# Optimization experiments

Measured on AMD Instinct MI355X. Metric: run time of the kernel, lower is better.

Reference implementation:

```python
import jax, jax.numpy as jnp
import numpy as np

N_NODES = 10000
N_EDGES = 80000
D = 512
L = 5
ALPHA = 0.1  # LeakyReLU slope inside GraphAttention
ACT_ALPHA = 0.1  # outer activation slope
EPS = 1e-5
W_SCALE = 0.05  # ~ xavier_normal gain 1.414 for fan_in+fan_out=1536


def leaky(x, a):
    return jnp.where(x >= 0, x, a * x)


def setup_inputs() -> dict:
    key = jax.random.key(0)
    ks = jax.random.split(key, 9)
    return {
        "node_feats": jax.random.normal(ks[0], (N_NODES, D), jnp.float32),
        "edge_feats": jax.random.normal(ks[1], (N_EDGES, D), jnp.float32),
        "src": jax.random.randint(ks[2], (N_EDGES,), 0, N_NODES, jnp.int32),
        "dst": jax.random.randint(ks[3], (N_EDGES,), 0, N_NODES, jnp.int32),
        "Wa": jax.random.normal(ks[4], (L, 2 * D, D), jnp.float32) * W_SCALE,
        "Wn": jax.random.normal(ks[5], (L, 2 * D, D), jnp.float32) * W_SCALE,
        "We": jax.random.normal(ks[6], (L, 2 * D, D), jnp.float32) * W_SCALE,
        "Wnc": jax.random.normal(ks[7], (D, 55), jnp.float32) * W_SCALE,
        "Wec": jax.random.normal(ks[8], (D, 2), jnp.float32) * W_SCALE,
    }


def reference(node_feats, edge_feats, src, dst, Wa, Wn, We, Wnc, Wec):
    n = node_feats.shape[0]
    nx, ex = node_feats, edge_feats
    for l in range(L):
        nx_src = nx[src]  # [E, D]
        nx_dst = nx[dst]  # [E, D]
        # a_p = exp(fa([e_x, dst_x]) - columnwise max over edges)
        ap = jnp.concatenate((ex, nx_dst), axis=1) @ Wa[l]
        ap = jnp.exp(ap - jnp.max(ap, axis=0, keepdims=True))
        # a_r = exp(fa([e_x, src_x]) - columnwise max over edges)
        ar = jnp.concatenate((ex, nx_src), axis=1) @ Wa[l]
        ar = jnp.exp(ar - jnp.max(ar, axis=0, keepdims=True))
        # softmax-like normalization per destination node
        z = jax.ops.segment_sum(ap, dst, num_segments=n)  # [N, D]
        a = ap / (z[dst] + EPS)
        # aggregate a * edge_x to destination nodes
        z2 = jax.ops.segment_sum(a * ex, dst, num_segments=n)  # [N, D]
        ft = jnp.concatenate((z2, nx), axis=1) @ Wn[l]
        # edge update: blend src/dst node feats by a_r/a_p shares
        a_sum = ap + ar
        blend = (ar / a_sum) * nx_src + (ap / a_sum) * nx_dst
        ex_new = jnp.concatenate((blend, ex), axis=1) @ We[l]
        # inner leaky_relu then outer activation (both LeakyReLU)
        nx = leaky(leaky(ft, ALPHA), ACT_ALPHA)
        ex = leaky(leaky(ex_new, ALPHA), ACT_ALPHA)
    node_conf = nx @ Wnc
    edge_conf = ex @ Wec
    return (nx, node_conf, ex, edge_conf)
```

## Files before the change

kernel.cpp:

```cpp
#include <hip/hip_runtime.h>
#include <hip/hip_fp16.h>
#include <math.h>

#define D 512
#define NNODES 10000
#define NEDGES 80000
#define LAYERS 5
#define EPS 1e-5f

typedef _Float16 f16x8 __attribute__((ext_vector_type(8)));
typedef float f32x4 __attribute__((ext_vector_type(4)));

__device__ inline unsigned short f2h(float x) { return __half_as_ushort(__float2half(x)); }
__device__ inline float h2f(unsigned short u) { return __half2float(__ushort_as_half(u)); }
__device__ inline uint4 pack8(const unsigned short* v) {
  uint4 r;
  r.x = (unsigned)v[0] | ((unsigned)v[1] << 16);
  r.y = (unsigned)v[2] | ((unsigned)v[3] << 16);
  r.z = (unsigned)v[4] | ((unsigned)v[5] << 16);
  r.w = (unsigned)v[6] | ((unsigned)v[7] << 16);
  return r;
}
__device__ inline void unpack8(uint4 v, unsigned short* o) {
  o[0] = v.x & 0xffff; o[1] = v.x >> 16;
  o[2] = v.y & 0xffff; o[3] = v.y >> 16;
  o[4] = v.z & 0xffff; o[5] = v.z >> 16;
  o[6] = v.w & 0xffff; o[7] = v.w >> 16;
}

__device__ inline void gload16(const void* g, void* l) {
  __builtin_amdgcn_global_load_lds((const __attribute__((address_space(1))) void*)g,
                                   (__attribute__((address_space(3))) void*)l, 16, 0, 0);
}

__device__ inline int octA(int r, int o) {
  return ((o >> 2) << 6) + ((((o & 3) ^ ((r >> 1) & 3))) << 4);
}

__global__ __launch_bounds__(256) void toF16_k(const float* __restrict__ src,
                                               char* __restrict__ dst, int nOct) {
  for (long long i = (long long)blockIdx.x * 256 + threadIdx.x; i < nOct;
       i += (long long)gridDim.x * 256) {
    int row = (int)(i >> 6), oct = (int)(i & 63);
    const float* s = src + (size_t)row * 512 + oct * 8;
    float4 x0 = *(const float4*)s, x1 = *(const float4*)(s + 4);
    float xs[8] = {x0.x, x0.y, x0.z, x0.w, x1.x, x1.y, x1.z, x1.w};
    unsigned short h[8];
#pragma unroll
    for (int j = 0; j < 8; j++) h[j] = f2h(xs[j]);
    *(uint4*)(dst + (size_t)row * 1024 + octA(row, oct)) = pack8(h);
  }
}

__global__ __launch_bounds__(256) void wprep_k(const float* __restrict__ Wa,
                                               const float* __restrict__ Wn,
                                               const float* __restrict__ We,
                                               char* __restrict__ WT) {
  __shared__ float tile[64][65];
  int mat = blockIdx.z;
  const float* W = (mat < 5) ? Wa + (size_t)mat * 1024 * 512
                 : (mat < 10) ? Wn + (size_t)(mat - 5) * 1024 * 512
                              : We + (size_t)(mat - 10) * 1024 * 512;
  char* out = WT + (size_t)mat * 512 * 2048;
  int n0 = blockIdx.x * 64, k0 = blockIdx.y * 64;
  int t = threadIdx.x;
  int ty = t >> 2, tx = t & 3;
  const float* wr = W + (size_t)(k0 + ty) * 512 + n0 + tx * 16;
  float4 v0 = *(const float4*)(wr + 0), v1 = *(const float4*)(wr + 4);
  float4 v2 = *(const float4*)(wr + 8), v3 = *(const float4*)(wr + 12);
  float vv[16] = {v0.x, v0.y, v0.z, v0.w, v1.x, v1.y, v1.z, v1.w,
                  v2.x, v2.y, v2.z, v2.w, v3.x, v3.y, v3.z, v3.w};
#pragma unroll
  for (int j = 0; j < 16; j++) tile[ty][tx * 16 + j] = vv[j];
  __syncthreads();
#pragma unroll
  for (int p = 0; p < 2; p++) {
    int chunk = t + p * 256;
    int n = chunk >> 3, cc = chunk & 7;
    float xs[8];
#pragma unroll
    for (int j = 0; j < 8; j++) xs[j] = tile[cc * 8 + j][n];
    unsigned short h[8];
#pragma unroll
    for (int j = 0; j < 8; j++) h[j] = f2h(xs[j]);
    int ng = n0 + n;
    int kc = (k0 >> 3) + cc;
    *(uint4*)(out + (size_t)ng * 2048 + octA(ng, kc)) = pack8(h);
  }
}

__global__ __launch_bounds__(256) void hist_k(const int* __restrict__ dst, int* __restrict__ cnt) {
  int e = blockIdx.x * 256 + threadIdx.x;
  if (e < NEDGES) atomicAdd(&cnt[dst[e]], 1);
}

__global__ __launch_bounds__(256) void scan_k(const int* __restrict__ cnt,
                                              int* __restrict__ off, int* __restrict__ cur) {
  __shared__ int part[256];
  const int CH = (NNODES + 255) / 256;
  int t = threadIdx.x;
  int s = 0;
  int l0 = t * CH;
  for (int i = 0; i < CH; i++) {
    int idx = l0 + i;
    if (idx < NNODES) s += cnt[idx];
  }
  part[t] = s;
  __syncthreads();
  if (t == 0) {
    int acc = 0;
    for (int i = 0; i < 256; i++) { int v = part[i]; part[i] = acc; acc += v; }
  }
  __syncthreads();
  int acc = part[t];
  for (int i = 0; i < CH; i++) {
    int idx = l0 + i;
    if (idx < NNODES) { off[idx] = acc; cur[idx] = acc; acc += cnt[idx]; }
  }
  if (t == 255) off[NNODES] = acc;
}

__global__ __launch_bounds__(256) void scatter_k(const int* __restrict__ dst,
                                                 int* __restrict__ cur, int* __restrict__ eid) {
  int e = blockIdx.x * 256 + threadIdx.x;
  if (e < NEDGES) {
    int p = atomicAdd(&cur[dst[e]], 1);
    eid[p] = e;
  }
}

template<int KT, bool ACT, bool OUT_I, bool CMAX>
__global__ __launch_bounds__(256) void gemmI(const char* __restrict__ X1,
                                             const char* __restrict__ X2,
                                             const char* __restrict__ BW, int cb0,
                                             void* __restrict__ Yout, int R,
                                             const int* __restrict__ srcI,
                                             const int* __restrict__ dstI,
                                             const float* __restrict__ Na,
                                             float* __restrict__ part_p,
                                             float* __restrict__ part_r) {
  __shared__ char smem[49152];
  const int tid = threadIdx.x;
  const int lane = tid & 63, wv = tid >> 6;
  const int NT = KT / 32;
  int flat = blockIdx.y * 4 + blockIdx.x;
  int total = gridDim.y * 4;
  int xcd = flat & 7, idx = flat >> 3;
  int q = total >> 3, rem = total & 7;
  int base = xcd * q + (xcd < rem ? xcd : rem);
  int f2 = base + idx;
  const int bn0 = (f2 & 3) * 128, bm0 = (f2 >> 2) * 128;
  const int r16 = lane & 15, g = lane >> 4;
  const int mo = (wv >> 1) * 64, no = (wv & 1) * 64;
  const int lr16 = lane >> 2, ls16 = (lane & 3) * 16;
  f32x4 acc[4][4];
#pragma unroll
  for (int i = 0; i < 4; i++)
#pragma unroll
    for (int j = 0; j < 4; j++) acc[i][j] = (f32x4){0.f, 0.f, 0.f, 0.f};

  int offA[4], offB[4];
#pragma unroll
  for (int mi = 0; mi < 4; mi++) {
    int row = mo + mi * 16 + r16;
    offA[mi] = row * 64 + ((g ^ ((row >> 1) & 3)) << 4);
  }
#pragma unroll
  for (int ni = 0; ni < 4; ni++) {
    int row = no + ni * 16 + r16;
    offB[ni] = row * 64 + ((g ^ ((row >> 1) & 3)) << 4);
  }

  const char* pA0;
  const char* pA1;
  const char* pB0;
  const char* pB1;
  {
    int g0 = bm0 + wv * 16 + lr16; if (g0 > R - 1) g0 = R - 1;
    int g1 = bm0 + (4 + wv) * 16 + lr16; if (g1 > R - 1) g1 = R - 1;
    pA0 = X1 + (size_t)g0 * 1024 + ls16;
    pA1 = X1 + (size_t)g1 * 1024 + ls16;
    int n0r = bn0 + wv * 16 + lr16;
    int n1r = bn0 + (4 + wv) * 16 + lr16;
    pB0 = BW + (size_t)n0r * 2048 + cb0 * 16 + ls16;
    pB1 = BW + (size_t)n1r * 2048 + cb0 * 16 + ls16;
  }

  int us = 0;
#define STAGE()                                                 \
  {                                                             \
    char* sb = smem + (us % 3) * 16384;                         \
    gload16(pA0, sb + wv * 1024);                               \
    gload16(pA1, sb + (4 + wv) * 1024);                         \
    gload16(pB0, sb + 8192 + wv * 1024);                        \
    gload16(pB1, sb + 8192 + (4 + wv) * 1024);                  \
    pA0 += 64; pA1 += 64; pB0 += 64; pB1 += 64;                 \
    us++;                                                       \
  }

  STAGE();
  STAGE();
  for (int t = 0; t < NT; ++t) {
    if (t + 1 < NT) {
      asm volatile("s_waitcnt vmcnt(4)" ::: "memory");
    } else {
      asm volatile("s_waitcnt vmcnt(0)" ::: "memory");
    }
    __builtin_amdgcn_s_barrier();
    if (us < NT) {
      if (KT == 1024 && us == 16) {
        int g0 = bm0 + wv * 16 + lr16; if (g0 > R - 1) g0 = R - 1;
        int g1 = bm0 + (4 + wv) * 16 + lr16; if (g1 > R - 1) g1 = R - 1;
        pA0 = X2 + (size_t)g0 * 1024 + ls16;
        pA1 = X2 + (size_t)g1 * 1024 + ls16;
      }
      STAGE();
    }
    const char* As = smem + (t % 3) * 16384;
    const char* Bs = As + 8192;
    f16x8 a[4], b[4];
#pragma unroll
    for (int mi = 0; mi < 4; mi++) a[mi] = *(const f16x8*)(As + offA[mi]);
#pragma unroll
    for (int ni = 0; ni < 4; ni++) b[ni] = *(const f16x8*)(Bs + offB[ni]);
    __builtin_amdgcn_s_setprio(1);
#pragma unroll
    for (int mi = 0; mi < 4; mi++)
#pragma unroll
      for (int ni = 0; ni < 4; ni++)
        acc[mi][ni] = __builtin_amdgcn_mfma_f32_16x16x32_f16(a[mi], b[ni], acc[mi][ni], 0, 0, 0);
    __builtin_amdgcn_s_setprio(0);
  }
#undef STAGE

  if (!OUT_I) {
    float* Y = (float*)Yout;
#pragma unroll
    for (int mi = 0; mi < 4; mi++)
#pragma unroll
      for (int j = 0; j < 4; j++) {
        int row = bm0 + mo + mi * 16 + g * 4 + j;
        if (row < R) {
#pragma unroll
          for (int ni = 0; ni < 4; ni++) {
            float v = acc[mi][ni][j];
            if (ACT) v = (v >= 0.f) ? v : 0.01f * v;
            Y[(size_t)row * 512 + bn0 + no + ni * 16 + r16] = v;
          }
        }
      }
  } else {
    float* stg = (float*)smem;
    const int rg = tid >> 5, cq = (tid & 31) * 4;
    float4 mp4 = make_float4(-1e30f, -1e30f, -1e30f, -1e30f);
    float4 mr4 = mp4;
#pragma unroll
    for (int h = 0; h < 2; h++) {
      __syncthreads();
      if ((wv >> 1) == h) {
#pragma unroll
        for (int mi = 0; mi < 4; mi++)
#pragma unroll
          for (int j = 0; j < 4; j++) {
            int rl = mi * 16 + g * 4 + j;
#pragma unroll
            for (int ni = 0; ni < 4; ni++) {
              float v = acc[mi][ni][j];
              if (ACT) v = (v >= 0.f) ? v : 0.01f * v;
              stg[rl * 128 + no + ni * 16 + r16] = v;
            }
          }
      }
      __syncthreads();
#pragma unroll
      for (int qq = 0; qq < 4; qq++) {
        int idx2 = tid + qq * 256;
        int rl = idx2 >> 4, oc = idx2 & 15;
        int grow = bm0 + h * 64 + rl;
        if (grow < R) {
          unsigned short hh[8];
#pragma unroll
          for (int j = 0; j < 8; j++) hh[j] = f2h(stg[rl * 128 + oc * 8 + j]);
          int oct = (bn0 >> 3) + oc;
          *(uint4*)((char*)Yout + (size_t)grow * 1024 + octA(grow, oct)) = pack8(hh);
        }
      }
      if (CMAX) {
#pragma unroll 2
        for (int r = rg * 8; r < rg * 8 + 8; r++) {
          int grow = bm0 + h * 64 + r;
          int d = dstI[grow], s = srcI[grow];
          float4 v = *(const float4*)&stg[r * 128 + cq];
          v.x = h2f(f2h(v.x)); v.y = h2f(f2h(v.y));
          v.z = h2f(f2h(v.z)); v.w = h2f(f2h(v.w));
          float4 nd = *(const float4*)&Na[(size_t)d * 512 + bn0 + cq];
          float4 ns = *(const float4*)&Na[(size_t)s * 512 + bn0 + cq];
          mp4.x = fmaxf(mp4.x, v.x + nd.x); mp4.y = fmaxf(mp4.y, v.y + nd.y);
          mp4.z = fmaxf(mp4.z, v.z + nd.z); mp4.w = fmaxf(mp4.w, v.w + nd.w);
          mr4.x = fmaxf(mr4.x, v.x + ns.x); mr4.y = fmaxf(mr4.y, v.y + ns.y);
          mr4.z = fmaxf(mr4.z, v.z + ns.z); mr4.w = fmaxf(mr4.w, v.w + ns.w);
        }
      }
    }
    if (CMAX) {
      __syncthreads();
      float* red = (float*)smem;
      *(float4*)&red[rg * 128 + cq] = mp4;
      *(float4*)&red[1024 + rg * 128 + cq] = mr4;
      __syncthreads();
      if (tid < 128) {
        float vp = -1e30f, vr = -1e30f;
#pragma unroll
        for (int gi = 0; gi < 8; gi++) {
          vp = fmaxf(vp, red[gi * 128 + tid]);
          vr = fmaxf(vr, red[1024 + gi * 128 + tid]);
        }
        int panel = f2 >> 2;
        part_p[(size_t)panel * 512 + bn0 + tid] = vp;
        part_r[(size_t)panel * 512 + bn0 + tid] = vr;
      }
    }
  }
}

__global__ __launch_bounds__(256) void colmax_red_k(const float* __restrict__ part,
                                                    float* __restrict__ m) {
  int idx = blockIdx.x * 256 + threadIdx.x;
  int c = idx & 511;
  const float* P = part + (size_t)(idx >> 9) * (625 * 512) + c;
  float v = -1e30f;
#pragma unroll 1
  for (int b = 0; b < 625; b += 5) {
    float v0 = P[(size_t)(b + 0) * 512], v1 = P[(size_t)(b + 1) * 512];
    float v2 = P[(size_t)(b + 2) * 512], v3 = P[(size_t)(b + 3) * 512];
    float v4 = P[(size_t)(b + 4) * 512];
    v = fmaxf(v, fmaxf(fmaxf(v0, v1), fmaxf(fmaxf(v2, v3), v4)));
  }
  m[idx] = v;
}

__global__ __launch_bounds__(256) void aggblend_k(const char* __restrict__ EaH,
                                                  const float* __restrict__ Na,
                                                  const char* __restrict__ exI,
                                                  const char* __restrict__ nxI,
                                                  const int* __restrict__ src,
                                                  const int* __restrict__ off,
                                                  const int* __restrict__ eid,
                                                  const float* __restrict__ mp,
                                                  const float* __restrict__ mr,
                                                  char* __restrict__ blendH,
                                                  char* __restrict__ z2I) {
  const int w = threadIdx.x >> 6, o = threadIdx.x & 63;
  int n = blockIdx.x * 4 + w;
  if (n >= NNODES) return;
  float m_p[8], m_r[8], nd[8], xd[8], z[8], z2[8];
#pragma unroll
  for (int j = 0; j < 8; j++) {
    m_p[j] = mp[o * 8 + j];
    m_r[j] = mr[o * 8 + j];
    z[j] = 0.f; z2[j] = 0.f;
  }
  {
    const float* np = Na + (size_t)n * 512 + o * 8;
    float4 d0 = *(const float4*)np, d1 = *(const float4*)(np + 4);
    nd[0] = d0.x; nd[1] = d0.y; nd[2] = d0.z; nd[3] = d0.w;
    nd[4] = d1.x; nd[5] = d1.y; nd[6] = d1.z; nd[7] = d1.w;
    unsigned short hh[8];
    unpack8(*(const uint4*)(nxI + (size_t)n * 1024 + octA(n, o)), hh);
#pragma unroll
    for (int j = 0; j < 8; j++) xd[j] = h2f(hh[j]);
  }
  const int i0 = off[n], i1 = off[n + 1];
  if (i0 < i1) {
    int e = eid[i0];
    int s = src[e];
    uint4 cea = *(const uint4*)(EaH + (size_t)e * 1024 + octA(e, o));
    const float* ns = Na + (size_t)s * 512 + o * 8;
    float4 cs0 = *(const float4*)ns, cs1 = *(const float4*)(ns + 4);
    uint4 cx = *(const uint4*)(exI + (size_t)e * 1024 + octA(e, o));
    uint4 cn = *(const uint4*)(nxI + (size_t)s * 1024 + octA(s, o));
    for (int i = i0; i < i1; i++) {
      int en = 0, sn = 0;
      float4 ps0, ps1;
      uint4 pea, px, pn;
      const bool more = (i + 1 < i1);
      if (more) {
        en = eid[i + 1];
        sn = src[en];
        pea = *(const uint4*)(EaH + (size_t)en * 1024 + octA(en, o));
        const float* ns2 = Na + (size_t)sn * 512 + o * 8;
        ps0 = *(const float4*)ns2; ps1 = *(const float4*)(ns2 + 4);
        px = *(const uint4*)(exI + (size_t)en * 1024 + octA(en, o));
        pn = *(const uint4*)(nxI + (size_t)sn * 1024 + octA(sn, o));
      }
      unsigned short eh[8], xh[8], sh[8];
      unpack8(cea, eh);
      unpack8(cx, xh);
      unpack8(cn, sh);
      float sv[8] = {cs0.x, cs0.y, cs0.z, cs0.w, cs1.x, cs1.y, cs1.z, cs1.w};
      unsigned short bh[8];
#pragma unroll
      for (int j = 0; j < 8; j++) {
        float ev = h2f(eh[j]);
        float sp = ev + nd[j] - m_p[j];
        float sr = ev + sv[j] - m_r[j];
        float ap = __expf(sp);
        float xe = h2f(xh[j]);
        z[j] += ap;
        z2[j] += ap * xe;
        float u = sr - sp;
        float evx = __expf(-fabsf(u));
        float wpos = 1.f / (1.f + evx);
        float wr = (u >= 0.f) ? wpos : 1.f - wpos;
        float xs_ = h2f(sh[j]);
        bh[j] = f2h(wr * xs_ + (1.f - wr) * xd[j]);
      }
      *(uint4*)(blendH + (size_t)e * 1024 + octA(e, o)) = pack8(bh);
      if (more) {
        e = en; s = sn;
        cea = pea; cs0 = ps0; cs1 = ps1;
        cx = px; cn = pn;
      }
    }
  }
  unsigned short zh[8];
#pragma unroll
  for (int j = 0; j < 8; j++) zh[j] = f2h(z2[j] / (z[j] + EPS));
  *(uint4*)(z2I + (size_t)n * 1024 + octA(n, o)) = pack8(zh);
}

__global__ __launch_bounds__(256) void nodeconf_k(const float* __restrict__ nx,
                                                  const float* __restrict__ Wnc,
                                                  float* __restrict__ out) {
  int w = threadIdx.x >> 6, lane = threadIdx.x & 63;
  int n = blockIdx.x * 4 + w;
  const float* r = nx + (size_t)n * D;
  if (lane < 55) {
    float acc = 0.f;
    for (int k = 0; k < D; k++) acc = fmaf(r[k], Wnc[k * 55 + lane], acc);
    out[(size_t)n * 55 + lane] = acc;
  }
}

__global__ __launch_bounds__(256) void edgeconf_k(const float* __restrict__ ex,
                                                  const float* __restrict__ Wec,
                                                  float* __restrict__ out) {
  int w = threadIdx.x >> 6, lane = threadIdx.x & 63;
  int e = blockIdx.x * 4 + w;
  const float* r = ex + (size_t)e * D;
  float a0 = 0.f, a1 = 0.f;
#pragma unroll
  for (int j = 0; j < 8; j++) {
    int c = lane + j * 64;
    float x = r[c];
    a0 = fmaf(x, Wec[c * 2 + 0], a0);
    a1 = fmaf(x, Wec[c * 2 + 1], a1);
  }
#pragma unroll
  for (int off = 32; off; off >>= 1) {
    a0 += __shfl_down(a0, off);
    a1 += __shfl_down(a1, off);
  }
  if (lane == 0) { out[(size_t)e * 2 + 0] = a0; out[(size_t)e * 2 + 1] = a1; }
}

extern "C" void kernel_launch(void* const* d_in, const int* in_sizes, int n_in,
                              void* d_out, int out_size, void* d_ws, size_t ws_size,
                              hipStream_t stream) {
  const float* in_nx = (const float*)d_in[0];
  const float* in_ex = (const float*)d_in[1];
  const int* src = (const int*)d_in[2];
  const int* dst = (const int*)d_in[3];
  const float* Wa = (const float*)d_in[4];
  const float* Wn = (const float*)d_in[5];
  const float* We = (const float*)d_in[6];
  const float* Wnc = (const float*)d_in[7];
  const float* Wec = (const float*)d_in[8];

  float* out = (float*)d_out;
  float* o_nx = out;
  float* o_nc = o_nx + (size_t)NNODES * D;
  float* o_ex = o_nc + (size_t)NNODES * 55;
  float* o_ec = o_ex + (size_t)NEDGES * D;

  const size_t SZ_EH = (size_t)NEDGES * 1024;
  const size_t SZ_NH = (size_t)NNODES * 1024;
  const size_t SZ_NF = (size_t)NNODES * 2048;
  const size_t MATSZ = (size_t)512 * 2048;
  char* w = (char*)d_ws;
  char* EaH = w;
  char* blendH = w + SZ_EH;
  char* exA = w + 2 * SZ_EH;
  char* nxA = w + 3 * SZ_EH;
  float* Na = (float*)(w + 3 * SZ_EH + SZ_NH);
  char* z2I = w + 3 * SZ_EH + SZ_NH + SZ_NF;
  float* mpf = (float*)(w + 3 * SZ_EH + 2 * SZ_NH + SZ_NF);
  char* WT = w + 3 * SZ_EH + 2 * SZ_NH + SZ_NF + 8192;
  char* csr = WT + 15 * MATSZ;
  int* cnt = (int*)csr;
  int* offp = cnt + NNODES + 8;
  int* cur = offp + NNODES + 8;
  int* eid = cur + NNODES + 8;
  float* part_p = (float*)(eid + NEDGES);
  float* part_r = part_p + 625 * 512;

  char* exB = (char*)o_ex;
  char* nxB = (char*)o_nx;

  wprep_k<<<dim3(8, 16, 15), 256, 0, stream>>>(Wa, Wn, We, WT);
  toF16_k<<<2048, 256, 0, stream>>>(in_ex, exA, NEDGES * 64);
  toF16_k<<<2048, 256, 0, stream>>>(in_nx, nxA, NNODES * 64);
  hipMemsetAsync(cnt, 0, NNODES * sizeof(int), stream);
  hist_k<<<(NEDGES + 255) / 256, 256, 0, stream>>>(dst, cnt);
  scan_k<<<1, 256, 0, stream>>>(cnt, offp, cur);
  scatter_k<<<(NEDGES + 255) / 256, 256, 0, stream>>>(dst, cur, eid);

  dim3 gE(4, NEDGES / 128);
  dim3 gN(4, (NNODES + 127) / 128);

  for (int l = 0; l < LAYERS; l++) {
    const char* WaT = WT + (size_t)l * MATSZ;
    const char* WnT = WT + (size_t)(5 + l) * MATSZ;
    const char* WeT = WT + (size_t)(10 + l) * MATSZ;
    char* exCur = (l & 1) ? exB : exA;
    char* exNxt = (l & 1) ? exA : exB;
    char* nxCur = (l & 1) ? nxB : nxA;
    char* nxNxt = (l & 1) ? nxA : nxB;

    gemmI<512, false, false, false><<<gN, 256, 0, stream>>>(
        nxCur, nullptr, WaT, 64, Na, NNODES, nullptr, nullptr, nullptr, nullptr, nullptr);
    gemmI<512, false, true, true><<<gE, 256, 0, stream>>>(
        exCur, nullptr, WaT, 0, EaH, NEDGES, src, dst, Na, part_p, part_r);

    colmax_red_k<<<4, 256, 0, stream>>>(part_p, mpf);

    aggblend_k<<<(NNODES + 3) / 4, 256, 0, stream>>>(EaH, Na, exCur, nxCur, src,
                                                     offp, eid, mpf, mpf + 512, blendH, z2I);

    if (l < 4)
      gemmI<1024, true, true, false><<<gN, 256, 0, stream>>>(
          z2I, nxCur, WnT, 0, nxNxt, NNODES, nullptr, nullptr, nullptr, nullptr, nullptr);
    else
      gemmI<1024, true, false, false><<<gN, 256, 0, stream>>>(
          z2I, nxCur, WnT, 0, o_nx, NNODES, nullptr, nullptr, nullptr, nullptr, nullptr);

    if (l < 4)
      gemmI<1024, true, true, false><<<gE, 256, 0, stream>>>(
          blendH, exCur, WeT, 0, exNxt, NEDGES, nullptr, nullptr, nullptr, nullptr, nullptr);
    else
      gemmI<1024, true, false, false><<<gE, 256, 0, stream>>>(
          blendH, exCur, WeT, 0, o_ex, NEDGES, nullptr, nullptr, nullptr, nullptr, nullptr);
  }

  nodeconf_k<<<NNODES / 4, 256, 0, stream>>>(o_nx, Wnc, o_nc);
  edgeconf_k<<<NEDGES / 4, 256, 0, stream>>>(o_ex, Wec, o_ec);
}
```

Before: 2.080 ms.

## Load GEMM B operand directly into registers and double-buffer A through LDS

Replaces the three-stage async global-to-LDS pipeline with register prefetching. Weight (B) fragments are now read straight from global memory into MFMA registers, using a non-swizzled weight layout. A tiles are staged through a two-buffer LDS ring using ordinary loads and stores, with a prefetch distance of two iterations. This cuts LDS traffic and shared-memory size, but adds register pressure and uncached, possibly uncoalesced global reads of weights per wave, and it drops the overlap the async LDS loads gave.

After: 2.685 ms. 1.29x slower.

```diff
diff --git a/kernel.cpp b/kernel.cpp
--- a/kernel.cpp
+++ b/kernel.cpp
@@ -26,11 +26,6 @@
   o[2] = v.y & 0xffff; o[3] = v.y >> 16;
   o[4] = v.z & 0xffff; o[5] = v.z >> 16;
   o[6] = v.w & 0xffff; o[7] = v.w >> 16;
-}
-
-__device__ inline void gload16(const void* g, void* l) {
-  __builtin_amdgcn_global_load_lds((const __attribute__((address_space(1))) void*)g,
-                                   (__attribute__((address_space(3))) void*)l, 16, 0, 0);
 }
 
 __device__ inline int octA(int r, int o) {
@@ -85,7 +80,7 @@
     for (int j = 0; j < 8; j++) h[j] = f2h(xs[j]);
     int ng = n0 + n;
     int kc = (k0 >> 3) + cc;
-    *(uint4*)(out + (size_t)ng * 2048 + octA(ng, kc)) = pack8(h);
+    *(uint4*)(out + (size_t)ng * 2048 + kc * 16) = pack8(h);
   }
 }
 
@@ -139,7 +134,7 @@
                                              const float* __restrict__ Na,
                                              float* __restrict__ part_p,
                                              float* __restrict__ part_r) {
-  __shared__ char smem[49152];
+  __shared__ char smem[32768];
   const int tid = threadIdx.x;
   const int lane = tid & 63, wv = tid >> 6;
   const int NT = KT / 32;
@@ -159,79 +154,88 @@
 #pragma unroll
     for (int j = 0; j < 4; j++) acc[i][j] = (f32x4){0.f, 0.f, 0.f, 0.f};
 
-  int offA[4], offB[4];
+  int offA[4];
 #pragma unroll
   for (int mi = 0; mi < 4; mi++) {
     int row = mo + mi * 16 + r16;
     offA[mi] = row * 64 + ((g ^ ((row >> 1) & 3)) << 4);
   }
-#pragma unroll
-  for (int ni = 0; ni < 4; ni++) {
-    int row = no + ni * 16 + r16;
-    offB[ni] = row * 64 + ((g ^ ((row >> 1) & 3)) << 4);
-  }
-
-  const char* pA0;
-  const char* pA1;
-  const char* pB0;
-  const char* pB1;
+  int g0 = bm0 + wv * 16 + lr16; if (g0 > R - 1) g0 = R - 1;
+  int g1 = bm0 + 64 + wv * 16 + lr16; if (g1 > R - 1) g1 = R - 1;
+  const char* a1_0 = X1 + (size_t)g0 * 1024 + ls16;
+  const char* a1_1 = X1 + (size_t)g1 * 1024 + ls16;
+  const char* a2_0 = (KT == 1024) ? X2 + (size_t)g0 * 1024 + ls16 : a1_0;
+  const char* a2_1 = (KT == 1024) ? X2 + (size_t)g1 * 1024 + ls16 : a1_1;
+  const char* pB[4];
+#pragma unroll
+  for (int ni = 0; ni < 4; ni++)
+    pB[ni] = BW + (size_t)(bn0 + no + ni * 16 + r16) * 2048 + cb0 * 16 + g * 16;
+  const int w0 = wv * 1024 + lane * 16;
+  const int w1 = (4 + wv) * 1024 + lane * 16;
+
   {
-    int g0 = bm0 + wv * 16 + lr16; if (g0 > R - 1) g0 = R - 1;
-    int g1 = bm0 + (4 + wv) * 16 + lr16; if (g1 > R - 1) g1 = R - 1;
-    pA0 = X1 + (size_t)g0 * 1024 + ls16;
-    pA1 = X1 + (size_t)g1 * 1024 + ls16;
-    int n0r = bn0 + wv * 16 + lr16;
-    int n1r = bn0 + (4 + wv) * 16 + lr16;
-    pB0 = BW + (size_t)n0r * 2048 + cb0 * 16 + ls16;
-    pB1 = BW + (size_t)n1r * 2048 + cb0 * 16 + ls16;
-  }
-
-  int us = 0;
-#define STAGE()                                                 \
-  {                                                             \
-    char* sb = smem + (us % 3) * 16384;                         \
-    gload16(pA0, sb + wv * 1024);                               \
-    gload16(pA1, sb + (4 + wv) * 1024);                         \
-    gload16(pB0, sb + 8192 + wv * 1024);                        \
-    gload16(pB1, sb + 8192 + (4 + wv) * 1024);                  \
-    pA0 += 64; pA1 += 64; pB0 += 64; pB1 += 64;                 \
-    us++;                                                       \
-  }
-
-  STAGE();
-  STAGE();
+    uint4 t00 = *(const uint4*)a1_0;
+    uint4 t01 = *(const uint4*)a1_1;
+    *(uint4*)(smem + w0) = t00;
+    *(uint4*)(smem + w1) = t01;
+  }
+  uint4 ah0, ah1;
+  {
+    const char* b0 = (KT == 1024 && NT <= 16) ? a1_0 : a1_0;
+    (void)b0;
+    ah0 = *(const uint4*)(a1_0 + 64);
+    ah1 = *(const uint4*)(a1_1 + 64);
+  }
+  f16x8 bc[4];
+#pragma unroll
+  for (int ni = 0; ni < 4; ni++) bc[ni] = *(const f16x8*)(pB[ni]);
+  asm volatile("s_waitcnt lgkmcnt(0)" ::: "memory");
+  __builtin_amdgcn_s_barrier();
+  __builtin_amdgcn_sched_barrier(0);
+
+#pragma unroll 4
   for (int t = 0; t < NT; ++t) {
+    f16x8 bn[4];
+    uint4 an0 = make_uint4(0, 0, 0, 0), an1 = make_uint4(0, 0, 0, 0);
     if (t + 1 < NT) {
-      asm volatile("s_waitcnt vmcnt(4)" ::: "memory");
+      int koff = (t + 1) * 64;
+#pragma unroll
+      for (int ni = 0; ni < 4; ni++) bn[ni] = *(const f16x8*)(pB[ni] + koff);
     } else {
-      asm volatile("s_waitcnt vmcnt(0)" ::: "memory");
+#pragma unroll
+      for (int ni = 0; ni < 4; ni++) bn[ni] = bc[ni];
     }
-    __builtin_amdgcn_s_barrier();
-    if (us < NT) {
-      if (KT == 1024 && us == 16) {
-        int g0 = bm0 + wv * 16 + lr16; if (g0 > R - 1) g0 = R - 1;
-        int g1 = bm0 + (4 + wv) * 16 + lr16; if (g1 > R - 1) g1 = R - 1;
-        pA0 = X2 + (size_t)g0 * 1024 + ls16;
-        pA1 = X2 + (size_t)g1 * 1024 + ls16;
-      }
-      STAGE();
+    if (t + 2 < NT) {
+      int t2 = t + 2;
+      const char* b0 = (KT == 1024 && t2 >= 16) ? a2_0 : a1_0;
+      const char* b1 = (KT == 1024 && t2 >= 16) ? a2_1 : a1_1;
+      int koff = (KT == 1024 ? (t2 & 15) : t2) * 64;
+      an0 = *(const uint4*)(b0 + koff);
+      an1 = *(const uint4*)(b1 + koff);
     }
-    const char* As = smem + (t % 3) * 16384;
-    const char* Bs = As + 8192;
-    f16x8 a[4], b[4];
+    const char* As = smem + (t & 1) * 8192;
+    f16x8 a[4];
 #pragma unroll
     for (int mi = 0; mi < 4; mi++) a[mi] = *(const f16x8*)(As + offA[mi]);
-#pragma unroll
-    for (int ni = 0; ni < 4; ni++) b[ni] = *(const f16x8*)(Bs + offB[ni]);
     __builtin_amdgcn_s_setprio(1);
 #pragma unroll
     for (int mi = 0; mi < 4; mi++)
 #pragma unroll
       for (int ni = 0; ni < 4; ni++)
-        acc[mi][ni] = __builtin_amdgcn_mfma_f32_16x16x32_f16(a[mi], b[ni], acc[mi][ni], 0, 0, 0);
+        acc[mi][ni] = __builtin_amdgcn_mfma_f32_16x16x32_f16(a[mi], bc[ni], acc[mi][ni], 0, 0, 0);
     __builtin_amdgcn_s_setprio(0);
-  }
-#undef STAGE
+    if (t + 1 < NT) {
+      char* wbuf = smem + ((t + 1) & 1) * 8192;
+      *(uint4*)(wbuf + w0) = ah0;
+      *(uint4*)(wbuf + w1) = ah1;
+      asm volatile("s_waitcnt lgkmcnt(0)" ::: "memory");
+      __builtin_amdgcn_s_barrier();
+      __builtin_amdgcn_sched_barrier(0);
+    }
+    ah0 = an0; ah1 = an1;
+#pragma unroll
+    for (int ni = 0; ni < 4; ni++) bc[ni] = bn[ni];
+  }
 
   if (!OUT_I) {
     float* Y = (float*)Yout;
@@ -286,7 +290,7 @@
         }
       }
       if (CMAX) {
-#pragma unroll 2
+#pragma unroll 4
         for (int r = rg * 8; r < rg * 8 + 8; r++) {
           int grow = bm0 + h * 64 + r;
           int d = dstI[grow], s = srcI[grow];
```

## Split column-max reduction, deepen aggblend prefetch, vectorize edgeconf loads

Applied to the files above, without the earlier changes.

The column-max reduction over 625 partial rows is split into two kernels: 20 blocks each reduce a segment of 125 rows, then a second kernel combines the 5 segment results. This addresses the original 4-block launch, which left most of the GPU idle. The aggblend edge loop now prefetches two edges ahead instead of one, to hide gather latency, at the cost of more registers. edgeconf switches to contiguous float4 loads per lane. Because the dot product is a sum, the changed mapping of columns to lanes is still correct.

Result: faster. 1.979 ms (-4.9%).

```diff
diff --git a/kernel.cpp b/kernel.cpp
--- a/kernel.cpp
+++ b/kernel.cpp
@@ -323,19 +323,31 @@
   }
 }
 
-__global__ __launch_bounds__(256) void colmax_red_k(const float* __restrict__ part,
-                                                    float* __restrict__ m) {
-  int idx = blockIdx.x * 256 + threadIdx.x;
+__global__ __launch_bounds__(256) void colmax_red1_k(const float* __restrict__ part,
+                                                     float* __restrict__ part2) {
+  int bx = blockIdx.x;
+  int seg = bx >> 2;
+  int idx = (bx & 3) * 256 + threadIdx.x;
   int c = idx & 511;
   const float* P = part + (size_t)(idx >> 9) * (625 * 512) + c;
+  int b0 = seg * 125, b1 = b0 + 125;
   float v = -1e30f;
 #pragma unroll 1
-  for (int b = 0; b < 625; b += 5) {
+  for (int b = b0; b < b1; b += 5) {
     float v0 = P[(size_t)(b + 0) * 512], v1 = P[(size_t)(b + 1) * 512];
     float v2 = P[(size_t)(b + 2) * 512], v3 = P[(size_t)(b + 3) * 512];
     float v4 = P[(size_t)(b + 4) * 512];
     v = fmaxf(v, fmaxf(fmaxf(v0, v1), fmaxf(fmaxf(v2, v3), v4)));
   }
+  part2[(size_t)seg * 1024 + idx] = v;
+}
+
+__global__ __launch_bounds__(256) void colmax_red2_k(const float* __restrict__ part2,
+                                                     float* __restrict__ m) {
+  int idx = blockIdx.x * 256 + threadIdx.x;
+  float v = part2[idx];
+#pragma unroll
+  for (int s = 1; s < 5; s++) v = fmaxf(v, part2[(size_t)s * 1024 + idx]);
   m[idx] = v;
 }
 
@@ -371,33 +383,40 @@
     for (int j = 0; j < 8; j++) xd[j] = h2f(hh[j]);
   }
   const int i0 = off[n], i1 = off[n + 1];
-  if (i0 < i1) {
-    int e = eid[i0];
-    int s = src[e];
-    uint4 cea = *(const uint4*)(EaH + (size_t)e * 1024 + octA(e, o));
-    const float* ns = Na + (size_t)s * 512 + o * 8;
-    float4 cs0 = *(const float4*)ns, cs1 = *(const float4*)(ns + 4);
-    uint4 cx = *(const uint4*)(exI + (size_t)e * 1024 + octA(e, o));
-    uint4 cn = *(const uint4*)(nxI + (size_t)s * 1024 + octA(s, o));
-    for (int i = i0; i < i1; i++) {
-      int en = 0, sn = 0;
-      float4 ps0, ps1;
-      uint4 pea, px, pn;
-      const bool more = (i + 1 < i1);
-      if (more) {
-        en = eid[i + 1];
-        sn = src[en];
-        pea = *(const uint4*)(EaH + (size_t)en * 1024 + octA(en, o));
-        const float* ns2 = Na + (size_t)sn * 512 + o * 8;
-        ps0 = *(const float4*)ns2; ps1 = *(const float4*)(ns2 + 4);
-        px = *(const uint4*)(exI + (size_t)en * 1024 + octA(en, o));
-        pn = *(const uint4*)(nxI + (size_t)sn * 1024 + octA(sn, o));
+  const int cnt = i1 - i0;
+  if (cnt > 0) {
+#define LOADE(ii, e_, ea_, x_, nn_, s0_, s1_)                        \
+    {                                                                \
+      e_ = eid[ii];                                                  \
+      int s_ = src[e_];                                              \
+      ea_ = *(const uint4*)(EaH + (size_t)e_ * 1024 + octA(e_, o));  \
+      x_  = *(const uint4*)(exI + (size_t)e_ * 1024 + octA(e_, o));  \
+      nn_ = *(const uint4*)(nxI + (size_t)s_ * 1024 + octA(s_, o));  \
+      const float* nsp_ = Na + (size_t)s_ * 512 + o * 8;             \
+      s0_ = *(const float4*)nsp_;                                    \
+      s1_ = *(const float4*)(nsp_ + 4);                              \
+    }
+    int eA, eB;
+    uint4 eaA, xA, nA, eaB, xB, nB;
+    float4 sA0, sA1, sB0, sB1;
+    LOADE(i0, eA, eaA, xA, nA, sA0, sA1);
+    if (cnt > 1) {
+      LOADE(i0 + 1, eB, eaB, xB, nB, sB0, sB1);
+    } else {
+      eB = eA; eaB = eaA; xB = xA; nB = nA; sB0 = sA0; sB1 = sA1;
+    }
+    for (int i = i0; i < i1; ++i) {
+      int eC = eB;
+      uint4 eaC = eaB, xC = xB, nC = nB;
+      float4 sC0 = sB0, sC1 = sB1;
+      if (i + 2 < i1) {
+        LOADE(i + 2, eC, eaC, xC, nC, sC0, sC1);
       }
       unsigned short eh[8], xh[8], sh[8];
-      unpack8(cea, eh);
-      unpack8(cx, xh);
-      unpack8(cn, sh);
-      float sv[8] = {cs0.x, cs0.y, cs0.z, cs0.w, cs1.x, cs1.y, cs1.z, cs1.w};
+      unpack8(eaA, eh);
+      unpack8(xA, xh);
+      unpack8(nA, sh);
+      float sv[8] = {sA0.x, sA0.y, sA0.z, sA0.w, sA1.x, sA1.y, sA1.z, sA1.w};
       unsigned short bh[8];
 #pragma unroll
       for (int j = 0; j < 8; j++) {
@@ -415,13 +434,11 @@
         float xs_ = h2f(sh[j]);
         bh[j] = f2h(wr * xs_ + (1.f - wr) * xd[j]);
       }
-      *(uint4*)(blendH + (size_t)e * 1024 + octA(e, o)) = pack8(bh);
-      if (more) {
-        e = en; s = sn;
-        cea = pea; cs0 = ps0; cs1 = ps1;
-        cx = px; cn = pn;
-      }
-    }
+      *(uint4*)(blendH + (size_t)eA * 1024 + octA(eA, o)) = pack8(bh);
+      eA = eB; eaA = eaB; xA = xB; nA = nB; sA0 = sB0; sA1 = sB1;
+      eB = eC; eaB = eaC; xB = xC; nB = nC; sB0 = sC0; sB1 = sC1;
+    }
+#undef LOADE
   }
   unsigned short zh[8];
 #pragma unroll
@@ -447,14 +464,16 @@
                                                   float* __restrict__ out) {
   int w = threadIdx.x >> 6, lane = threadIdx.x & 63;
   int e = blockIdx.x * 4 + w;
-  const float* r = ex + (size_t)e * D;
+  const float* r = ex + (size_t)e * D + lane * 8;
+  float4 v0 = *(const float4*)r;
+  float4 v1 = *(const float4*)(r + 4);
+  const float* wp = Wec + lane * 16;
+  float vv[8] = {v0.x, v0.y, v0.z, v0.w, v1.x, v1.y, v1.z, v1.w};
   float a0 = 0.f, a1 = 0.f;
 #pragma unroll
   for (int j = 0; j < 8; j++) {
-    int c = lane + j * 64;
-    float x = r[c];
-    a0 = fmaf(x, Wec[c * 2 + 0], a0);
-    a1 = fmaf(x, Wec[c * 2 + 1], a1);
+    a0 = fmaf(vv[j], wp[j * 2 + 0], a0);
+    a1 = fmaf(vv[j], wp[j * 2 + 1], a1);
   }
 #pragma unroll
   for (int off = 32; off; off >>= 1) {
@@ -503,6 +522,7 @@
   int* eid = cur + NNODES + 8;
   float* part_p = (float*)(eid + NEDGES);
   float* part_r = part_p + 625 * 512;
+  float* part2 = part_r + 625 * 512;
 
   char* exB = (char*)o_ex;
   char* nxB = (char*)o_nx;
@@ -532,7 +552,8 @@
     gemmI<512, false, true, true><<<gE, 256, 0, stream>>>(
         exCur, nullptr, WaT, 0, EaH, NEDGES, src, dst, Na, part_p, part_r);
 
-    colmax_red_k<<<4, 256, 0, stream>>>(part_p, mpf);
+    colmax_red1_k<<<20, 256, 0, stream>>>(part_p, part2);
+    colmax_red2_k<<<4, 256, 0, stream>>>(part2, mpf);
 
     aggblend_k<<<(NNODES + 3) / 4, 256, 0, stream>>>(EaH, Na, exCur, nxCur, src,
                                                      offp, eid, mpf, mpf + 512, blendH, z2I);
```
